# Optimization experiments

Measured on AMD Instinct MI355X. Metric: run time of the kernel, lower is better.

## Reference

```python
import jax, jax.numpy as jnp
import numpy as np

N, E, D, T = 100000, 1600000, 128, 5
EPS = 1e-5


def setup_inputs() -> dict:
    key = jax.random.key(0)
    ks = jax.random.split(key, 8)
    scale = 1.0 / np.sqrt(D)
    return {
        "features": jax.random.normal(ks[0], (N, D), dtype=jnp.float32),
        "src": jax.random.randint(ks[1], (E,), 0, N, dtype=jnp.int32),
        "dst": jax.random.randint(ks[2], (E,), 0, N, dtype=jnp.int32),
        "etype": jax.random.randint(ks[3], (E,), 0, T, dtype=jnp.int32),
        "w1": jax.random.normal(ks[4], (T * D, D), dtype=jnp.float32) * scale,
        "b1": jnp.zeros((T * D,), dtype=jnp.float32),
        "g1": jnp.ones((D,), dtype=jnp.float32),
        "be1": jnp.zeros((D,), dtype=jnp.float32),
        "w2": jax.random.normal(ks[5], (T * D, D), dtype=jnp.float32) * scale,
        "b2": jnp.zeros((T * D,), dtype=jnp.float32),
        "g2": jnp.ones((D,), dtype=jnp.float32),
        "be2": jnp.zeros((D,), dtype=jnp.float32),
    }


def _bn(x, gamma, beta):
    # BatchNorm1d in training mode: biased batch statistics over node axis.
    mu = jnp.mean(x, axis=0)
    var = jnp.mean((x - mu) ** 2, axis=0)
    return gamma * (x - mu) * jax.lax.rsqrt(var + EPS) + beta


def _round(x, w, b, gamma, beta, src, dst, etype):
    h = jax.nn.relu(_bn(x, gamma, beta))
    h = jnp.einsum('nd,od->no', h, w) + b          # [N, T*D]
    h3 = h.reshape(N, T, D)
    # one-hot multiply + sum over types == select the etype slice per edge
    msg = h3[src, etype]                            # [E, D] gather
    return jax.ops.segment_sum(msg, dst, num_segments=N)  # [N, D] scatter-add


def reference(features, src, dst, etype, w1, b1, g1, be1, w2, b2, g2, be2):
    h_new = _round(features, w1, b1, g1, be1, src, dst, etype)
    h_new = _round(h_new, w2, b2, g2, be2, src, dst, etype)
    return h_new + features
```

## Files before the change

### kernel.cpp

```cpp
#include <hip/hip_runtime.h>

#define NN 100000
#define EE 1600000
#define DD 128
#define TD 640
#define EPSV 1e-5f
#define NBLK_SCAN 391

typedef __attribute__((ext_vector_type(8))) short bf16x8;
typedef __attribute__((ext_vector_type(4))) float f32x4;

__device__ inline unsigned short f2b(float f) {
  union { float f; unsigned u; } x; x.f = f;
  unsigned r = x.u + 0x7fff + ((x.u >> 16) & 1);
  return (unsigned short)(r >> 16);
}
__device__ inline float b2f(unsigned short u) {
  union { unsigned u; float f; } x; x.u = ((unsigned)u) << 16;
  return x.f;
}

__global__ __launch_bounds__(256) void k_stats_partial(const float* __restrict__ x,
    float* __restrict__ ps, float* __restrict__ pq) {
  __shared__ float ls[256], lq[256];
  int t = threadIdx.x;
  int col = t & 127, sub = t >> 7;
  float s = 0.f, q = 0.f;
  for (int r = blockIdx.x * 2 + sub; r < NN; r += 512) {
    float v = x[r * DD + col];
    s += v; q += v * v;
  }
  ls[t] = s; lq[t] = q;
  __syncthreads();
  if (t < 128) {
    ps[blockIdx.x * DD + t] = ls[t] + ls[t + 128];
    pq[blockIdx.x * DD + t] = lq[t] + lq[t + 128];
  }
}

__global__ void k_stats_final(const float* __restrict__ ps, const float* __restrict__ pq,
    const float* __restrict__ g, const float* __restrict__ be, float* __restrict__ ssb) {
  int c = threadIdx.x;
  float s = 0.f, q = 0.f;
  for (int b = 0; b < 256; ++b) { s += ps[b * DD + c]; q += pq[b * DD + c]; }
  float mean = s * (1.0f / NN);
  float var  = q * (1.0f / NN) - mean * mean;
  float sc = g[c] * rsqrtf(var + EPSV);
  ssb[c] = sc;
  ssb[DD + c] = be[c] - mean * sc;
}

__global__ __launch_bounds__(256) void k_act(const float* __restrict__ x,
    const float* __restrict__ ss, unsigned short* __restrict__ A) {
  int i = blockIdx.x * 256 + threadIdx.x;
  float4 v = reinterpret_cast<const float4*>(x)[i];
  int c4 = (i & 31) * 4;
  float s0 = ss[c4+0], s1 = ss[c4+1], s2 = ss[c4+2], s3 = ss[c4+3];
  float h0 = ss[DD+c4+0], h1 = ss[DD+c4+1], h2 = ss[DD+c4+2], h3 = ss[DD+c4+3];
  ushort4 o;
  o.x = f2b(fmaxf(0.f, v.x * s0 + h0));
  o.y = f2b(fmaxf(0.f, v.y * s1 + h1));
  o.z = f2b(fmaxf(0.f, v.z * s2 + h2));
  o.w = f2b(fmaxf(0.f, v.w * s3 + h3));
  reinterpret_cast<ushort4*>(A)[i] = o;
}

__global__ void k_cvt(const float* __restrict__ w, unsigned short* __restrict__ o) {
  int i = blockIdx.x * 256 + threadIdx.x;
  float4 v = reinterpret_cast<const float4*>(w)[i];
  ushort4 u; u.x = f2b(v.x); u.y = f2b(v.y); u.z = f2b(v.z); u.w = f2b(v.w);
  reinterpret_cast<ushort4*>(o)[i] = u;
}

__global__ void k_zero(int* p, int n) {
  int i = blockIdx.x * 256 + threadIdx.x;
  if (i < n) p[i] = 0;
}
__global__ void k_hist(const int* __restrict__ dst, int* __restrict__ cnt) {
  int i = blockIdx.x * 256 + threadIdx.x;
  if (i < EE) atomicAdd(&cnt[dst[i]], 1);
}
__global__ __launch_bounds__(256) void k_scan_blk(const int* __restrict__ cnt, int* __restrict__ bsum) {
  __shared__ int sh[256];
  int idx = blockIdx.x * 256 + threadIdx.x;
  sh[threadIdx.x] = (idx < NN) ? cnt[idx] : 0;
  __syncthreads();
  for (int off = 128; off > 0; off >>= 1) {
    if (threadIdx.x < off) sh[threadIdx.x] += sh[threadIdx.x + off];
    __syncthreads();
  }
  if (threadIdx.x == 0) bsum[blockIdx.x] = sh[0];
}
__global__ __launch_bounds__(512) void k_scan_top(int* __restrict__ bsum) {
  __shared__ int sh[512];
  int t = threadIdx.x;
  int v = (t < NBLK_SCAN) ? bsum[t] : 0;
  sh[t] = v;
  __syncthreads();
  for (int off = 1; off < 512; off <<= 1) {
    int add = (t >= off) ? sh[t - off] : 0;
    __syncthreads();
    sh[t] += add;
    __syncthreads();
  }
  if (t < NBLK_SCAN) bsum[t] = sh[t] - v;
}
__global__ __launch_bounds__(256) void k_scan_fin(const int* __restrict__ cnt,
    const int* __restrict__ bsum, int* __restrict__ row_ptr, int* __restrict__ cursor) {
  __shared__ int sh[256];
  int idx = blockIdx.x * 256 + threadIdx.x;
  int v = (idx < NN) ? cnt[idx] : 0;
  sh[threadIdx.x] = v;
  __syncthreads();
  for (int off = 1; off < 256; off <<= 1) {
    int add = (threadIdx.x >= off) ? sh[threadIdx.x - off] : 0;
    __syncthreads();
    sh[threadIdx.x] += add;
    __syncthreads();
  }
  int excl = bsum[blockIdx.x] + sh[threadIdx.x] - v;
  if (idx < NN) { row_ptr[idx] = excl; cursor[idx] = excl; }
  if (idx == NN - 1) row_ptr[NN] = excl + v;
}
__global__ void k_scatter(const int* __restrict__ src, const int* __restrict__ dst,
    const int* __restrict__ et, int* __restrict__ cursor, int* __restrict__ payload) {
  int i = blockIdx.x * 256 + threadIdx.x;
  if (i < EE) {
    int pos = atomicAdd(&cursor[dst[i]], 1);
    payload[pos] = (src[i] << 3) | et[i];
  }
}

__global__ __launch_bounds__(256) void k_gemm(const unsigned short* __restrict__ A,
    const unsigned short* __restrict__ W, const float* __restrict__ bias,
    unsigned short* __restrict__ H) {
  const int l = threadIdx.x & 63;
  const int w = threadIdx.x >> 6;
  const int C = blockIdx.y * 64;
  const int lm = l & 15;
  const int lk = (l >> 4) * 8;

  bf16x8 bfr[4][4];
#pragma unroll
  for (int kk = 0; kk < 4; ++kk)
#pragma unroll
    for (int f = 0; f < 4; ++f)
      bfr[kk][f] = *reinterpret_cast<const bf16x8*>(W + (C + f * 16 + lm) * DD + kk * 32 + lk);

  float bv[4];
#pragma unroll
  for (int f = 0; f < 4; ++f) bv[f] = bias[C + f * 16 + lm];

  const int NT = 1563;
  for (int tile = blockIdx.x; tile < NT; tile += gridDim.x) {
    const int R = tile * 64 + w * 16;
    int arow = R + lm; if (arow >= NN) arow = NN - 1;
    const unsigned short* aptr = A + arow * DD + lk;
    f32x4 acc[4] = {};
#pragma unroll
    for (int kk = 0; kk < 4; ++kk) {
      bf16x8 af = *reinterpret_cast<const bf16x8*>(aptr + kk * 32);
#pragma unroll
      for (int f = 0; f < 4; ++f)
        acc[f] = __builtin_amdgcn_mfma_f32_16x16x32_bf16(af, bfr[kk][f], acc[f], 0, 0, 0);
    }
    const int r0 = R + (l >> 4) * 4;
#pragma unroll
    for (int f = 0; f < 4; ++f) {
      int col = C + f * 16 + lm;
#pragma unroll
      for (int r = 0; r < 4; ++r) {
        int row = r0 + r;
        if (row < NN) H[row * TD + col] = f2b(acc[f][r] + bv[f]);
      }
    }
  }
}

__global__ __launch_bounds__(64) void k_gather(const unsigned short* __restrict__ H,
    const int* __restrict__ rp, const int* __restrict__ pl,
    const float* __restrict__ base, float* __restrict__ y) {
  int m = blockIdx.x;
  int l = threadIdx.x;
  int s = rp[m], e = rp[m + 1];
  float a0 = 0.f, a1 = 0.f;
  if (base) {
    float2 b = reinterpret_cast<const float2*>(base)[m * 64 + l];
    a0 = b.x; a1 = b.y;
  }
  int j = s;
  for (; j + 1 < e; j += 2) {
    int p0 = pl[j], p1 = pl[j + 1];
    ushort2 u0 = reinterpret_cast<const ushort2*>(H + (p0 >> 3) * TD + (p0 & 7) * DD)[l];
    ushort2 u1 = reinterpret_cast<const ushort2*>(H + (p1 >> 3) * TD + (p1 & 7) * DD)[l];
    a0 += b2f(u0.x) + b2f(u1.x);
    a1 += b2f(u0.y) + b2f(u1.y);
  }
  if (j < e) {
    int p0 = pl[j];
    ushort2 u0 = reinterpret_cast<const ushort2*>(H + (p0 >> 3) * TD + (p0 & 7) * DD)[l];
    a0 += b2f(u0.x);
    a1 += b2f(u0.y);
  }
  float2 o; o.x = a0; o.y = a1;
  reinterpret_cast<float2*>(y)[m * 64 + l] = o;
}

extern "C" void kernel_launch(void* const* d_in, const int* in_sizes, int n_in,
                              void* d_out, int out_size, void* d_ws, size_t ws_size,
                              hipStream_t stream) {
  const float* features = (const float*)d_in[0];
  const int*   src   = (const int*)d_in[1];
  const int*   dst   = (const int*)d_in[2];
  const int*   etype = (const int*)d_in[3];
  const float* w1  = (const float*)d_in[4];
  const float* b1  = (const float*)d_in[5];
  const float* g1  = (const float*)d_in[6];
  const float* be1 = (const float*)d_in[7];
  const float* w2  = (const float*)d_in[8];
  const float* b2  = (const float*)d_in[9];
  const float* g2  = (const float*)d_in[10];
  const float* be2 = (const float*)d_in[11];

  char* ws = (char*)d_ws;
  unsigned short* Ab   = (unsigned short*)(ws + 0);
  unsigned short* Hb   = (unsigned short*)(ws + 25600000);
  float*          y1   = (float*)(ws + 153600000);
  unsigned short* w1b  = (unsigned short*)(ws + 204800000);
  unsigned short* w2b  = (unsigned short*)(ws + 204963840);
  float*          ssb  = (float*)(ws + 205127680);
  float*          ps   = (float*)(ws + 205128704);
  float*          pq   = (float*)(ws + 205259776);
  int*            rowp = (int*)(ws + 205390848);
  int*            curs = (int*)(ws + 205790864);
  int*            payl = (int*)(ws + 206190864);
  int*            bsum = (int*)(ws + 212590864);

  k_zero<<<(NN + 255) / 256, 256, 0, stream>>>(curs, NN);
  k_hist<<<(EE + 255) / 256, 256, 0, stream>>>(dst, curs);
  k_scan_blk<<<NBLK_SCAN, 256, 0, stream>>>(curs, bsum);
  k_scan_top<<<1, 512, 0, stream>>>(bsum);
  k_scan_fin<<<NBLK_SCAN, 256, 0, stream>>>(curs, bsum, rowp, curs);
  k_scatter<<<(EE + 255) / 256, 256, 0, stream>>>(src, dst, etype, curs, payl);

  k_cvt<<<80, 256, 0, stream>>>(w1, w1b);
  k_cvt<<<80, 256, 0, stream>>>(w2, w2b);

  dim3 gemm_grid(391, 10);

  k_stats_partial<<<256, 256, 0, stream>>>(features, ps, pq);
  k_stats_final<<<1, 128, 0, stream>>>(ps, pq, g1, be1, ssb);
  k_act<<<12500, 256, 0, stream>>>(features, ssb, Ab);
  k_gemm<<<gemm_grid, 256, 0, stream>>>(Ab, w1b, b1, Hb);
  k_gather<<<NN, 64, 0, stream>>>(Hb, rowp, payl, nullptr, y1);

  k_stats_partial<<<256, 256, 0, stream>>>(y1, ps, pq);
  k_stats_final<<<1, 128, 0, stream>>>(ps, pq, g2, be2, ssb);
  k_act<<<12500, 256, 0, stream>>>(y1, ssb, Ab);
  k_gemm<<<gemm_grid, 256, 0, stream>>>(Ab, w2b, b2, Hb);
  k_gather<<<NN, 64, 0, stream>>>(Hb, rowp, payl, features, (float*)d_out);
}
```

Measured before the change: 617.6 us.

## Vectorize BN stats, widen GEMM grid with row-contiguous stores, nontemporal payload

BN statistics now use float4 loads over 1024 blocks with a two-level reduction in a 1024-thread final kernel, with partials stored in the A buffer region. The GEMM drops its persistent tile loop for one tile per block, swaps MFMA operands so each lane owns a row, and writes four contiguous bf16 outputs with float4 bias loads. The CSR scatter uses nontemporal stores for the payload. This trades more block launches and reused workspace for wider, coalesced memory traffic.

```diff
diff --git a/kernel.cpp b/kernel.cpp
--- a/kernel.cpp
+++ b/kernel.cpp
@@ -6,6 +6,7 @@
 #define TD 640
 #define EPSV 1e-5f
 #define NBLK_SCAN 391
+#define SB 1024
 
 typedef __attribute__((ext_vector_type(8))) short bf16x8;
 typedef __attribute__((ext_vector_type(4))) float f32x4;
@@ -22,32 +23,51 @@
 
 __global__ __launch_bounds__(256) void k_stats_partial(const float* __restrict__ x,
     float* __restrict__ ps, float* __restrict__ pq) {
+  float s0=0.f,s1=0.f,s2=0.f,s3=0.f,q0=0.f,q1=0.f,q2=0.f,q3=0.f;
+  const float4* x4 = reinterpret_cast<const float4*>(x);
+  const int total = NN * DD / 4;
+  for (int i = blockIdx.x * 256 + threadIdx.x; i < total; i += SB * 256) {
+    float4 v = x4[i];
+    s0 += v.x; s1 += v.y; s2 += v.z; s3 += v.w;
+    q0 += v.x*v.x; q1 += v.y*v.y; q2 += v.z*v.z; q3 += v.w*v.w;
+  }
   __shared__ float ls[256], lq[256];
   int t = threadIdx.x;
-  int col = t & 127, sub = t >> 7;
+  float sv[4] = {s0,s1,s2,s3}, qv[4] = {q0,q1,q2,q3};
+#pragma unroll
+  for (int j = 0; j < 4; ++j) {
+    ls[t] = sv[j]; lq[t] = qv[j];
+    __syncthreads();
+    if (t < 32) {
+      float a = 0.f, b = 0.f;
+#pragma unroll
+      for (int k = 0; k < 8; ++k) { a += ls[t + 32*k]; b += lq[t + 32*k]; }
+      ps[blockIdx.x * DD + t*4 + j] = a;
+      pq[blockIdx.x * DD + t*4 + j] = b;
+    }
+    __syncthreads();
+  }
+}
+
+__global__ __launch_bounds__(1024) void k_stats_final(const float* __restrict__ ps,
+    const float* __restrict__ pq, const float* __restrict__ g,
+    const float* __restrict__ be, float* __restrict__ ssb) {
+  __shared__ float ls[1024], lq[1024];
+  int t = threadIdx.x;
+  int col = t & 127, seg = t >> 7;
   float s = 0.f, q = 0.f;
-  for (int r = blockIdx.x * 2 + sub; r < NN; r += 512) {
-    float v = x[r * DD + col];
-    s += v; q += v * v;
-  }
+  for (int b = seg; b < SB; b += 8) { s += ps[b * DD + col]; q += pq[b * DD + col]; }
   ls[t] = s; lq[t] = q;
   __syncthreads();
   if (t < 128) {
-    ps[blockIdx.x * DD + t] = ls[t] + ls[t + 128];
-    pq[blockIdx.x * DD + t] = lq[t] + lq[t + 128];
-  }
-}
-
-__global__ void k_stats_final(const float* __restrict__ ps, const float* __restrict__ pq,
-    const float* __restrict__ g, const float* __restrict__ be, float* __restrict__ ssb) {
-  int c = threadIdx.x;
-  float s = 0.f, q = 0.f;
-  for (int b = 0; b < 256; ++b) { s += ps[b * DD + c]; q += pq[b * DD + c]; }
-  float mean = s * (1.0f / NN);
-  float var  = q * (1.0f / NN) - mean * mean;
-  float sc = g[c] * rsqrtf(var + EPSV);
-  ssb[c] = sc;
-  ssb[DD + c] = be[c] - mean * sc;
+#pragma unroll
+    for (int k = 1; k < 8; ++k) { s += ls[t + 128*k]; q += lq[t + 128*k]; }
+    float mean = s * (1.0f / NN);
+    float var  = q * (1.0f / NN) - mean * mean;
+    float sc = g[t] * rsqrtf(var + EPSV);
+    ssb[t] = sc;
+    ssb[DD + t] = be[t] - mean * sc;
+  }
 }
 
 __global__ __launch_bounds__(256) void k_act(const float* __restrict__ x,
@@ -127,7 +147,7 @@
   int i = blockIdx.x * 256 + threadIdx.x;
   if (i < EE) {
     int pos = atomicAdd(&cursor[dst[i]], 1);
-    payload[pos] = (src[i] << 3) | et[i];
+    __builtin_nontemporal_store((src[i] << 3) | et[i], &payload[pos]);
   }
 }
 
@@ -138,7 +158,8 @@
   const int w = threadIdx.x >> 6;
   const int C = blockIdx.y * 64;
   const int lm = l & 15;
-  const int lk = (l >> 4) * 8;
+  const int hi = l >> 4;
+  const int lk = hi * 8;
 
   bf16x8 bfr[4][4];
 #pragma unroll
@@ -147,32 +168,33 @@
     for (int f = 0; f < 4; ++f)
       bfr[kk][f] = *reinterpret_cast<const bf16x8*>(W + (C + f * 16 + lm) * DD + kk * 32 + lk);
 
-  float bv[4];
-#pragma unroll
-  for (int f = 0; f < 4; ++f) bv[f] = bias[C + f * 16 + lm];
-
-  const int NT = 1563;
-  for (int tile = blockIdx.x; tile < NT; tile += gridDim.x) {
-    const int R = tile * 64 + w * 16;
-    int arow = R + lm; if (arow >= NN) arow = NN - 1;
-    const unsigned short* aptr = A + arow * DD + lk;
-    f32x4 acc[4] = {};
-#pragma unroll
-    for (int kk = 0; kk < 4; ++kk) {
-      bf16x8 af = *reinterpret_cast<const bf16x8*>(aptr + kk * 32);
-#pragma unroll
-      for (int f = 0; f < 4; ++f)
-        acc[f] = __builtin_amdgcn_mfma_f32_16x16x32_bf16(af, bfr[kk][f], acc[f], 0, 0, 0);
-    }
-    const int r0 = R + (l >> 4) * 4;
+  float4 bv[4];
+#pragma unroll
+  for (int f = 0; f < 4; ++f)
+    bv[f] = *reinterpret_cast<const float4*>(bias + C + f * 16 + hi * 4);
+
+  const int R = blockIdx.x * 64 + w * 16;
+  int arow = R + lm; if (arow >= NN) arow = NN - 1;
+  const unsigned short* aptr = A + arow * DD + lk;
+  f32x4 acc[4] = {};
+#pragma unroll
+  for (int kk = 0; kk < 4; ++kk) {
+    bf16x8 af = *reinterpret_cast<const bf16x8*>(aptr + kk * 32);
+#pragma unroll
+    for (int f = 0; f < 4; ++f)
+      acc[f] = __builtin_amdgcn_mfma_f32_16x16x32_bf16(bfr[kk][f], af, acc[f], 0, 0, 0);
+  }
+  const int n = R + lm;
+  if (n < NN) {
+    unsigned short* hp = H + n * TD + C + hi * 4;
 #pragma unroll
     for (int f = 0; f < 4; ++f) {
-      int col = C + f * 16 + lm;
-#pragma unroll
-      for (int r = 0; r < 4; ++r) {
-        int row = r0 + r;
-        if (row < NN) H[row * TD + col] = f2b(acc[f][r] + bv[f]);
-      }
+      ushort4 o;
+      o.x = f2b(acc[f][0] + bv[f].x);
+      o.y = f2b(acc[f][1] + bv[f].y);
+      o.z = f2b(acc[f][2] + bv[f].z);
+      o.w = f2b(acc[f][3] + bv[f].w);
+      *reinterpret_cast<ushort4*>(hp + f * 16) = o;
     }
   }
 }
@@ -224,13 +246,13 @@
 
   char* ws = (char*)d_ws;
   unsigned short* Ab   = (unsigned short*)(ws + 0);
+  float*          ps   = (float*)(ws + 0);
+  float*          pq   = (float*)(ws + 524288);
   unsigned short* Hb   = (unsigned short*)(ws + 25600000);
   float*          y1   = (float*)(ws + 153600000);
   unsigned short* w1b  = (unsigned short*)(ws + 204800000);
   unsigned short* w2b  = (unsigned short*)(ws + 204963840);
   float*          ssb  = (float*)(ws + 205127680);
-  float*          ps   = (float*)(ws + 205128704);
-  float*          pq   = (float*)(ws + 205259776);
   int*            rowp = (int*)(ws + 205390848);
   int*            curs = (int*)(ws + 205790864);
   int*            payl = (int*)(ws + 206190864);
@@ -246,16 +268,16 @@
   k_cvt<<<80, 256, 0, stream>>>(w1, w1b);
   k_cvt<<<80, 256, 0, stream>>>(w2, w2b);
 
-  dim3 gemm_grid(391, 10);
-
-  k_stats_partial<<<256, 256, 0, stream>>>(features, ps, pq);
-  k_stats_final<<<1, 128, 0, stream>>>(ps, pq, g1, be1, ssb);
+  dim3 gemm_grid(1563, 10);
+
+  k_stats_partial<<<SB, 256, 0, stream>>>(features, ps, pq);
+  k_stats_final<<<1, 1024, 0, stream>>>(ps, pq, g1, be1, ssb);
   k_act<<<12500, 256, 0, stream>>>(features, ssb, Ab);
   k_gemm<<<gemm_grid, 256, 0, stream>>>(Ab, w1b, b1, Hb);
   k_gather<<<NN, 64, 0, stream>>>(Hb, rowp, payl, nullptr, y1);
 
-  k_stats_partial<<<256, 256, 0, stream>>>(y1, ps, pq);
-  k_stats_final<<<1, 128, 0, stream>>>(ps, pq, g2, be2, ssb);
+  k_stats_partial<<<SB, 256, 0, stream>>>(y1, ps, pq);
+  k_stats_final<<<1, 1024, 0, stream>>>(ps, pq, g2, be2, ssb);
   k_act<<<12500, 256, 0, stream>>>(y1, ssb, Ab);
   k_gemm<<<gemm_grid, 256, 0, stream>>>(Ab, w2b, b2, Hb);
   k_gather<<<NN, 64, 0, stream>>>(Hb, rowp, payl, features, (float*)d_out);
```

Result: slower. 795.5 us (+28.8%).
